# Optimization experiments

Measured on AMD Instinct MI355X. Metric: run time of the kernel, lower is better.

Reference implementation:

```python
import jax, jax.numpy as jnp
import numpy as np

N_NODES = 50000
N_EDGES = 600000
N_GRAPHS = 256
IN_C = 128
HID = 128
OUT_C = 2


def setup_inputs() -> dict:
    key = jax.random.key(0)
    ks = jax.random.split(key, 16)
    d = {}
    d["x"] = jax.random.normal(ks[0], (N_NODES, IN_C), jnp.float32)
    d["edge_index"] = jax.random.randint(ks[1], (2, N_EDGES), 0, N_NODES, dtype=jnp.int32)
    d["root_node_idx"] = jax.random.randint(ks[2], (N_GRAPHS,), 0, N_NODES, dtype=jnp.int32)
    d["batch"] = jnp.sort(jax.random.randint(ks[3], (N_NODES,), 0, N_GRAPHS, dtype=jnp.int32))
    dims = [(IN_C, HID), (HID, HID), (HID, HID), (HID, HID)]
    for i, (ci, co) in enumerate(dims, start=1):
        s = 1.0 / np.sqrt(ci)
        d[f"w{i}_l"] = jax.random.uniform(ks[3 + i], (co, ci), jnp.float32, -s, s)
        d[f"b{i}_l"] = jnp.zeros((co,), jnp.float32)
        d[f"w{i}_r"] = jax.random.uniform(ks[7 + i], (co, ci), jnp.float32, -s, s)
    s = 1.0 / np.sqrt(2 * HID)
    d["w_cls"] = jax.random.uniform(ks[12], (OUT_C, 2 * HID), jnp.float32, -s, s)
    d["b_cls"] = jnp.zeros((OUT_C,), jnp.float32)
    return d


def _sage_conv(x, src, tgt, deg_inv, w_l, b_l, w_r):
    # mean aggregation of source features at target nodes (PyG SAGEConv, aggr='mean')
    agg = jax.ops.segment_sum(x[src], tgt, num_segments=N_NODES) * deg_inv  # [N, C]
    # out = lin_l(agg) + lin_r(x); lin_r has no bias in PyG SAGEConv
    return agg @ w_l.T + b_l + x @ w_r.T


def reference(x, edge_index, root_node_idx, batch,
              w1_l, b1_l, w1_r, w2_l, b2_l, w2_r,
              w3_l, b3_l, w3_r, w4_l, b4_l, w4_r,
              w_cls, b_cls):
    src, tgt = edge_index[0], edge_index[1]
    ones_e = jnp.ones((src.shape[0],), x.dtype)
    deg = jax.ops.segment_sum(ones_e, tgt, num_segments=N_NODES)
    deg_inv = (1.0 / jnp.maximum(deg, 1.0))[:, None]  # [N, 1]

    h = jax.nn.relu(_sage_conv(x, src, tgt, deg_inv, w1_l, b1_l, w1_r))
    h = jax.nn.relu(_sage_conv(h, src, tgt, deg_inv, w2_l, b2_l, w2_r))
    h = jax.nn.relu(_sage_conv(h, src, tgt, deg_inv, w3_l, b3_l, w3_r))
    h = jax.nn.relu(_sage_conv(h, src, tgt, deg_inv, w4_l, b4_l, w4_r))

    root_emb = h[root_node_idx]  # [G, HID]
    g_sum = jax.ops.segment_sum(h, batch, num_segments=N_GRAPHS)
    g_cnt = jax.ops.segment_sum(jnp.ones((h.shape[0],), h.dtype), batch, num_segments=N_GRAPHS)
    graph_emb = g_sum / jnp.maximum(g_cnt, 1.0)[:, None]  # [G, HID]

    combined = jnp.concatenate([root_emb, graph_emb], axis=1)  # [G, 2*HID]
    return combined @ w_cls.T + b_cls  # [G, OUT_C]
```

## Files before the change

kernel.cpp:

```cpp
#include <hip/hip_runtime.h>

#define N_NODES 50000
#define N_EDGES 600000
#define N_GRAPHS 256
#define C 128
#define NB 196
#define PB_DEG 2344
#define PB_WS  512

typedef unsigned short ushort;
typedef unsigned int uint;
typedef __attribute__((ext_vector_type(8))) short bfrag8;
typedef __attribute__((ext_vector_type(4))) float facc4;

__device__ __forceinline__ ushort f2bf(float v) {
    uint u = __float_as_uint(v);
    u += 0x7FFFu + ((u >> 16) & 1u);
    return (ushort)(u >> 16);
}
__device__ __forceinline__ float bf2f(ushort u) {
    return __uint_as_float(((uint)u) << 16);
}
__device__ __forceinline__ void fsplit(float v, ushort& h, ushort& l) {
    h = f2bf(v);
    l = f2bf(v - bf2f(h));
}

struct WPtrs { const float* wl[4]; const float* wr[4]; };

__global__ __launch_bounds__(256) void k_prep(const int* __restrict__ tgt,
                                              int* __restrict__ deg,
                                              WPtrs wp,
                                              ushort* __restrict__ BTh,
                                              ushort* __restrict__ BTl,
                                              const int* __restrict__ batch,
                                              int* __restrict__ gstart) {
    const int b = blockIdx.x, t = threadIdx.x;
    if (b < PB_DEG) {
        int e = b * 256 + t;
        if (e < N_EDGES) atomicAdd(&deg[tgt[e]], 1);
    } else if (b < PB_DEG + PB_WS) {
        int gid = (b - PB_DEG) * 256 + t;
        int l = gid >> 15;
        int rem = gid & 32767;
        int n = rem >> 8, k = rem & 255;
        float v = (k < 128) ? wp.wl[l][n * 128 + k] : wp.wr[l][n * 128 + (k - 128)];
        ushort h, lo;
        fsplit(v, h, lo);
        BTh[gid] = h;
        BTl[gid] = lo;
    } else {
        int g = t;
        int lo = 0, hi = N_NODES;
        while (lo < hi) {
            int mid = (lo + hi) >> 1;
            if (batch[mid] < g) lo = mid + 1;
            else hi = mid;
        }
        gstart[g] = lo;
        if (t == 0) gstart[N_GRAPHS] = N_NODES;
    }
}

__global__ __launch_bounds__(256) void k_scan1(const int* __restrict__ deg,
                                               int* __restrict__ bsum,
                                               float* __restrict__ dinv) {
    __shared__ int ws[4];
    int idx = blockIdx.x * 256 + threadIdx.x;
    int v = (idx < N_NODES) ? deg[idx] : 0;
    if (idx < N_NODES) dinv[idx] = 1.0f / fmaxf((float)v, 1.0f);
    int s = v;
#pragma unroll
    for (int off = 1; off < 64; off <<= 1) s += __shfl_xor(s, off);
    if ((threadIdx.x & 63) == 0) ws[threadIdx.x >> 6] = s;
    __syncthreads();
    if (threadIdx.x == 0) bsum[blockIdx.x] = ws[0] + ws[1] + ws[2] + ws[3];
}

__global__ __launch_bounds__(256) void k_scan2(const int* __restrict__ deg,
                                               const int* __restrict__ bsum,
                                               int* __restrict__ rowptr) {
    __shared__ int red[4];
    __shared__ int ws[4];
    const int b = blockIdx.x, t = threadIdx.x;
    const int lane = t & 63, w = t >> 6;
    int bv = (t < NB && t < b) ? bsum[t] : 0;
#pragma unroll
    for (int off = 1; off < 64; off <<= 1) bv += __shfl_xor(bv, off);
    if (lane == 0) red[w] = bv;
    __syncthreads();
    const int boff = red[0] + red[1] + red[2] + red[3];
    int idx = b * 256 + t;
    int v = (idx < N_NODES) ? deg[idx] : 0;
    int incl = v;
#pragma unroll
    for (int off = 1; off < 64; off <<= 1) {
        int u = __shfl_up(incl, off);
        if (lane >= off) incl += u;
    }
    if (lane == 63) ws[w] = incl;
    __syncthreads();
    int wo = 0;
    if (w > 0) wo += ws[0];
    if (w > 1) wo += ws[1];
    if (w > 2) wo += ws[2];
    if (idx < N_NODES) rowptr[idx] = boff + wo + incl - v;
    if (b == 0 && t == 0) rowptr[N_NODES] = N_EDGES;
}

__global__ void k_fill(const int* __restrict__ src, const int* __restrict__ tgt,
                       const int* __restrict__ rowptr, int* __restrict__ fill,
                       int* __restrict__ csr_src) {
    int e = blockIdx.x * blockDim.x + threadIdx.x;
    if (e >= N_EDGES) return;
    int d = tgt[e];
    int pos = atomicAdd(&fill[d], 1);
    csr_src[rowptr[d] + pos] = src[e];
}

__global__ __launch_bounds__(256) void k_gather(const float* __restrict__ Hsrc,
                                                ushort* __restrict__ AGhi,
                                                ushort* __restrict__ AGlo,
                                                const int* __restrict__ csr_src,
                                                const int* __restrict__ rowptr,
                                                const float* __restrict__ dinv) {
    int node = blockIdx.x * 8 + (threadIdx.x >> 5);
    if (node >= N_NODES) return;
    int lane = threadIdx.x & 31;
    int c4 = lane << 2;
    int s = rowptr[node], e = rowptr[node + 1];
    float sc = dinv[node];
    float a0 = 0.f, a1 = 0.f, a2 = 0.f, a3 = 0.f;
    int j = s;
    for (; j + 3 < e; j += 4) {
        int s0 = csr_src[j], s1 = csr_src[j + 1];
        int s2 = csr_src[j + 2], s3 = csr_src[j + 3];
        float4 v0 = *(const float4*)(Hsrc + (size_t)s0 * 128 + c4);
        float4 v1 = *(const float4*)(Hsrc + (size_t)s1 * 128 + c4);
        float4 v2 = *(const float4*)(Hsrc + (size_t)s2 * 128 + c4);
        float4 v3 = *(const float4*)(Hsrc + (size_t)s3 * 128 + c4);
        a0 += (v0.x + v1.x) + (v2.x + v3.x);
        a1 += (v0.y + v1.y) + (v2.y + v3.y);
        a2 += (v0.z + v1.z) + (v2.z + v3.z);
        a3 += (v0.w + v1.w) + (v2.w + v3.w);
    }
    for (; j < e; j++) {
        int s0 = csr_src[j];
        float4 v0 = *(const float4*)(Hsrc + (size_t)s0 * 128 + c4);
        a0 += v0.x; a1 += v0.y; a2 += v0.z; a3 += v0.w;
    }
    a0 *= sc; a1 *= sc; a2 *= sc; a3 *= sc;
    ushort4 h, l;
    fsplit(a0, h.x, l.x); fsplit(a1, h.y, l.y);
    fsplit(a2, h.z, l.z); fsplit(a3, h.w, l.w);
    *(ushort4*)(AGhi + (size_t)node * 128 + c4) = h;
    *(ushort4*)(AGlo + (size_t)node * 128 + c4) = l;
}

__global__ __launch_bounds__(512) void k_gemm(const ushort* __restrict__ AGhi,
                                              const ushort* __restrict__ AGlo,
                                              const float* __restrict__ Hsrc,
                                              const ushort* __restrict__ BTh,
                                              const ushort* __restrict__ BTl,
                                              const float* __restrict__ bl,
                                              float* __restrict__ Hout) {
    __shared__ short As[2][128][40];
    __shared__ short Bs[2][128][40];
    const int tid = threadIdx.x;
    const int wave = tid >> 6, lane = tid & 63;
    const int m0 = blockIdx.x * 128;
    const int wm = (wave & 1) * 64;
    const int wn = (wave >> 1) * 32;
    const int l15 = lane & 15, lk = (lane >> 4) * 8;

    const int sr = tid >> 2;
    const int sc = (tid & 3) * 8;
    int garow = m0 + sr; if (garow >= N_NODES) garow = N_NODES - 1;
    const ushort* pAh = AGhi + (size_t)garow * 128 + sc;
    const ushort* pAl = AGlo + (size_t)garow * 128 + sc;
    const float*  pHf = Hsrc + (size_t)garow * 128 + sc;
    const ushort* pBh = BTh + sr * 256 + sc;
    const ushort* pBl = BTl + sr * 256 + sc;

    bfrag8 rAh, rAl, rBh, rBl;
    float4 f0, f1;
#define LOADSTEP(S) do { \
        if ((S) < 4) { \
            rAh = *(const bfrag8*)(pAh + (S) * 32); \
            rAl = *(const bfrag8*)(pAl + (S) * 32); \
        } else { \
            f0 = *(const float4*)(pHf + ((S) - 4) * 32); \
            f1 = *(const float4*)(pHf + ((S) - 4) * 32 + 4); \
        } \
        rBh = *(const bfrag8*)(pBh + (S) * 32); \
        rBl = *(const bfrag8*)(pBl + (S) * 32); \
    } while (0)

    LOADSTEP(0);
    facc4 acc[4][2] = {};
#pragma unroll
    for (int s = 0; s < 8; s++) {
        if (s < 4) {
            *(bfrag8*)&As[0][sr][sc] = rAh;
            *(bfrag8*)&As[1][sr][sc] = rAl;
        } else {
            float v[8] = {f0.x, f0.y, f0.z, f0.w, f1.x, f1.y, f1.z, f1.w};
            bfrag8 Hh, Ll;
#pragma unroll
            for (int i = 0; i < 8; i++) {
                ushort hh, ll;
                fsplit(v[i], hh, ll);
                Hh[i] = (short)hh; Ll[i] = (short)ll;
            }
            *(bfrag8*)&As[0][sr][sc] = Hh;
            *(bfrag8*)&As[1][sr][sc] = Ll;
        }
        *(bfrag8*)&Bs[0][sr][sc] = rBh;
        *(bfrag8*)&Bs[1][sr][sc] = rBl;
        __syncthreads();
        if (s < 7) LOADSTEP(s + 1);
        bfrag8 a[2][4], b[2][2];
#pragma unroll
        for (int t = 0; t < 4; t++) {
            a[0][t] = *(const bfrag8*)&As[0][wm + t * 16 + l15][lk];
            a[1][t] = *(const bfrag8*)&As[1][wm + t * 16 + l15][lk];
        }
#pragma unroll
        for (int t = 0; t < 2; t++) {
            b[0][t] = *(const bfrag8*)&Bs[0][wn + t * 16 + l15][lk];
            b[1][t] = *(const bfrag8*)&Bs[1][wn + t * 16 + l15][lk];
        }
#pragma unroll
        for (int mt = 0; mt < 4; mt++)
#pragma unroll
            for (int nt = 0; nt < 2; nt++) {
                acc[mt][nt] = __builtin_amdgcn_mfma_f32_16x16x32_bf16(a[0][mt], b[0][nt], acc[mt][nt], 0, 0, 0);
                acc[mt][nt] = __builtin_amdgcn_mfma_f32_16x16x32_bf16(a[0][mt], b[1][nt], acc[mt][nt], 0, 0, 0);
                acc[mt][nt] = __builtin_amdgcn_mfma_f32_16x16x32_bf16(a[1][mt], b[0][nt], acc[mt][nt], 0, 0, 0);
            }
        __syncthreads();
    }
#undef LOADSTEP

    const int r4 = (lane >> 4) * 4;
#pragma unroll
    for (int mt = 0; mt < 4; mt++) {
#pragma unroll
        for (int nt = 0; nt < 2; nt++) {
            int col = wn + nt * 16 + l15;
            float bias = bl[col];
#pragma unroll
            for (int r = 0; r < 4; r++) {
                int grow = m0 + wm + mt * 16 + r4 + r;
                if (grow < N_NODES) {
                    Hout[(size_t)grow * 128 + col] = fmaxf(acc[mt][nt][r] + bias, 0.f);
                }
            }
        }
    }
}

__global__ __launch_bounds__(256) void k_head(const float* __restrict__ H,
                                              const int* __restrict__ gstart,
                                              const int* __restrict__ root,
                                              const float* __restrict__ wcls,
                                              const float* __restrict__ bcls,
                                              float* __restrict__ out) {
    __shared__ float gm[128];
    __shared__ float part[128];
    __shared__ float red[8];
    const int g = blockIdx.x, t = threadIdx.x;
    const int c = t & 127, p = t >> 7;
    int s = gstart[g], e = gstart[g + 1];
    float sum = 0.f;
    for (int n = s + p; n < e; n += 2) {
        sum += H[(size_t)n * 128 + c];
    }
    if (p) part[c] = sum;
    __syncthreads();
    if (!p) gm[c] = (sum + part[c]) / fmaxf((float)(e - s), 1.0f);
    __syncthreads();
    float v;
    if (t < 128) {
        v = H[(size_t)root[g] * 128 + t];
    } else {
        v = gm[t - 128];
    }
    float p0 = v * wcls[t];
    float p1 = v * wcls[256 + t];
#pragma unroll
    for (int off = 32; off; off >>= 1) {
        p0 += __shfl_down(p0, off);
        p1 += __shfl_down(p1, off);
    }
    int wid = t >> 6;
    if ((t & 63) == 0) { red[wid] = p0; red[4 + wid] = p1; }
    __syncthreads();
    if (t == 0) {
        out[g * 2 + 0] = red[0] + red[1] + red[2] + red[3] + bcls[0];
        out[g * 2 + 1] = red[4] + red[5] + red[6] + red[7] + bcls[1];
    }
}

extern "C" void kernel_launch(void* const* d_in, const int* in_sizes, int n_in,
                              void* d_out, int out_size, void* d_ws, size_t ws_size,
                              hipStream_t stream) {
    const float* x = (const float*)d_in[0];
    const int* ei = (const int*)d_in[1];
    const int* src = ei;
    const int* tgt = ei + N_EDGES;
    const int* root = (const int*)d_in[2];
    const int* batch = (const int*)d_in[3];
    WPtrs wp;
    wp.wl[0] = (const float*)d_in[4];  wp.wr[0] = (const float*)d_in[6];
    wp.wl[1] = (const float*)d_in[7];  wp.wr[1] = (const float*)d_in[9];
    wp.wl[2] = (const float*)d_in[10]; wp.wr[2] = (const float*)d_in[12];
    wp.wl[3] = (const float*)d_in[13]; wp.wr[3] = (const float*)d_in[15];
    const float* blv[4] = {(const float*)d_in[5], (const float*)d_in[8],
                           (const float*)d_in[11], (const float*)d_in[14]};
    const float* wcls = (const float*)d_in[16];
    const float* bcls = (const float*)d_in[17];
    float* out = (float*)d_out;

    float* H = (float*)d_ws;
    ushort* AGhi = (ushort*)(H + (size_t)N_NODES * 128);
    ushort* AGlo = AGhi + (size_t)N_NODES * 128;
    ushort* BTh = AGlo + (size_t)N_NODES * 128;
    ushort* BTl = BTh + 4 * 128 * 256;
    int* deg = (int*)(BTl + 4 * 128 * 256);
    int* fill = deg + N_NODES;
    float* dinv = (float*)(fill + N_NODES);
    int* rowptr = (int*)(dinv + N_NODES);
    int* csr_src = rowptr + N_NODES + 1;
    int* bsum = csr_src + N_EDGES;
    int* gstart = bsum + 256;

    hipMemsetAsync(deg, 0, 2 * N_NODES * sizeof(int), stream);
    k_prep<<<PB_DEG + PB_WS + 1, 256, 0, stream>>>(
        tgt, deg, wp, BTh, BTl, batch, gstart);
    k_scan1<<<NB, 256, 0, stream>>>(deg, bsum, dinv);
    k_scan2<<<NB, 256, 0, stream>>>(deg, bsum, rowptr);
    k_fill<<<(N_EDGES + 255) / 256, 256, 0, stream>>>(src, tgt, rowptr, fill, csr_src);

    for (int l = 0; l < 4; l++) {
        const float* hsrc = (l == 0) ? x : H;
        k_gather<<<(N_NODES + 7) / 8, 256, 0, stream>>>(hsrc, AGhi, AGlo,
                                                        csr_src, rowptr, dinv);
        k_gemm<<<(N_NODES + 127) / 128, 512, 0, stream>>>(
            AGhi, AGlo, hsrc, BTh + l * 32768, BTl + l * 32768, blv[l], H);
    }
    k_head<<<N_GRAPHS, 256, 0, stream>>>(H, gstart, root, wcls, bcls, out);
}
```

Measured before the change: 449.5 us.

## Split neighbor gather into four column-slice passes and store fp32 aggregates

The gather now runs as four launches, each covering a 32-column slice (128 bytes per row) with 8 threads per node. The aim is a smaller random-access working set per pass that fits better in cache. The gather writes fp32 aggregates instead of pre-split bf16 hi/lo halves, and the GEMM does the split for both operands. This adds three kernel launches per layer and reads csr_src four times. It also gives each gather access a smaller transaction and shifts conversion work into the GEMM.

```diff
diff --git a/kernel.cpp b/kernel.cpp
--- a/kernel.cpp
+++ b/kernel.cpp
@@ -118,16 +118,16 @@
     csr_src[rowptr[d] + pos] = src[e];
 }
 
-__global__ __launch_bounds__(256) void k_gather(const float* __restrict__ Hsrc,
-                                                ushort* __restrict__ AGhi,
-                                                ushort* __restrict__ AGlo,
-                                                const int* __restrict__ csr_src,
-                                                const int* __restrict__ rowptr,
-                                                const float* __restrict__ dinv) {
-    int node = blockIdx.x * 8 + (threadIdx.x >> 5);
+__global__ __launch_bounds__(256) void k_gather32(const float* __restrict__ Hsrc,
+                                                  float* __restrict__ AGf,
+                                                  const int* __restrict__ csr_src,
+                                                  const int* __restrict__ rowptr,
+                                                  const float* __restrict__ dinv,
+                                                  int c0) {
+    int node = blockIdx.x * 32 + (threadIdx.x >> 3);
     if (node >= N_NODES) return;
-    int lane = threadIdx.x & 31;
-    int c4 = lane << 2;
+    int lane = threadIdx.x & 7;
+    int c4 = c0 + (lane << 2);
     int s = rowptr[node], e = rowptr[node + 1];
     float sc = dinv[node];
     float a0 = 0.f, a1 = 0.f, a2 = 0.f, a3 = 0.f;
@@ -149,16 +149,11 @@
         float4 v0 = *(const float4*)(Hsrc + (size_t)s0 * 128 + c4);
         a0 += v0.x; a1 += v0.y; a2 += v0.z; a3 += v0.w;
     }
-    a0 *= sc; a1 *= sc; a2 *= sc; a3 *= sc;
-    ushort4 h, l;
-    fsplit(a0, h.x, l.x); fsplit(a1, h.y, l.y);
-    fsplit(a2, h.z, l.z); fsplit(a3, h.w, l.w);
-    *(ushort4*)(AGhi + (size_t)node * 128 + c4) = h;
-    *(ushort4*)(AGlo + (size_t)node * 128 + c4) = l;
-}
-
-__global__ __launch_bounds__(512) void k_gemm(const ushort* __restrict__ AGhi,
-                                              const ushort* __restrict__ AGlo,
+    float4 r; r.x = a0 * sc; r.y = a1 * sc; r.z = a2 * sc; r.w = a3 * sc;
+    *(float4*)(AGf + (size_t)node * 128 + c4) = r;
+}
+
+__global__ __launch_bounds__(512) void k_gemm(const float* __restrict__ AGf,
                                               const float* __restrict__ Hsrc,
                                               const ushort* __restrict__ BTh,
                                               const ushort* __restrict__ BTl,
@@ -176,22 +171,17 @@
     const int sr = tid >> 2;
     const int sc = (tid & 3) * 8;
     int garow = m0 + sr; if (garow >= N_NODES) garow = N_NODES - 1;
-    const ushort* pAh = AGhi + (size_t)garow * 128 + sc;
-    const ushort* pAl = AGlo + (size_t)garow * 128 + sc;
+    const float*  pAg = AGf  + (size_t)garow * 128 + sc;
     const float*  pHf = Hsrc + (size_t)garow * 128 + sc;
     const ushort* pBh = BTh + sr * 256 + sc;
     const ushort* pBl = BTl + sr * 256 + sc;
 
-    bfrag8 rAh, rAl, rBh, rBl;
+    bfrag8 rBh, rBl;
     float4 f0, f1;
 #define LOADSTEP(S) do { \
-        if ((S) < 4) { \
-            rAh = *(const bfrag8*)(pAh + (S) * 32); \
-            rAl = *(const bfrag8*)(pAl + (S) * 32); \
-        } else { \
-            f0 = *(const float4*)(pHf + ((S) - 4) * 32); \
-            f1 = *(const float4*)(pHf + ((S) - 4) * 32 + 4); \
-        } \
+        const float* pa = ((S) < 4) ? pAg : pHf; \
+        f0 = *(const float4*)(pa + ((S) & 3) * 32); \
+        f1 = *(const float4*)(pa + ((S) & 3) * 32 + 4); \
         rBh = *(const bfrag8*)(pBh + (S) * 32); \
         rBl = *(const bfrag8*)(pBl + (S) * 32); \
     } while (0)
@@ -200,10 +190,7 @@
     facc4 acc[4][2] = {};
 #pragma unroll
     for (int s = 0; s < 8; s++) {
-        if (s < 4) {
-            *(bfrag8*)&As[0][sr][sc] = rAh;
-            *(bfrag8*)&As[1][sr][sc] = rAl;
-        } else {
+        {
             float v[8] = {f0.x, f0.y, f0.z, f0.w, f1.x, f1.y, f1.z, f1.w};
             bfrag8 Hh, Ll;
 #pragma unroll
@@ -323,9 +310,8 @@
     float* out = (float*)d_out;
 
     float* H = (float*)d_ws;
-    ushort* AGhi = (ushort*)(H + (size_t)N_NODES * 128);
-    ushort* AGlo = AGhi + (size_t)N_NODES * 128;
-    ushort* BTh = AGlo + (size_t)N_NODES * 128;
+    float* AGf = H + (size_t)N_NODES * 128;
+    ushort* BTh = (ushort*)(AGf + (size_t)N_NODES * 128);
     ushort* BTl = BTh + 4 * 128 * 256;
     int* deg = (int*)(BTl + 4 * 128 * 256);
     int* fill = deg + N_NODES;
@@ -342,12 +328,14 @@
     k_scan2<<<NB, 256, 0, stream>>>(deg, bsum, rowptr);
     k_fill<<<(N_EDGES + 255) / 256, 256, 0, stream>>>(src, tgt, rowptr, fill, csr_src);
 
+    const int GB = (N_NODES + 31) / 32;
     for (int l = 0; l < 4; l++) {
         const float* hsrc = (l == 0) ? x : H;
-        k_gather<<<(N_NODES + 7) / 8, 256, 0, stream>>>(hsrc, AGhi, AGlo,
-                                                        csr_src, rowptr, dinv);
+        for (int p = 0; p < 4; p++) {
+            k_gather32<<<GB, 256, 0, stream>>>(hsrc, AGf, csr_src, rowptr, dinv, p * 32);
+        }
         k_gemm<<<(N_NODES + 127) / 128, 512, 0, stream>>>(
-            AGhi, AGlo, hsrc, BTh + l * 32768, BTl + l * 32768, blv[l], H);
+            AGf, hsrc, BTh + l * 32768, BTl + l * 32768, blv[l], H);
     }
     k_head<<<N_GRAPHS, 256, 0, stream>>>(H, gstart, root, wcls, bcls, out);
 }
```

Result: slower. 478.9 us (+6.6%).
